# Optimization experiments

Hardware: AMD Instinct MI355X
Metric: run time of the kernel (lower is better)

## Reference

```python
import jax, jax.numpy as jnp
import numpy as np
from itertools import product

N_CODONS = 2
ORDER = 2
N_STATES = 25          # calc_number_of_states() with nCodons=2
ALPHA6 = 6             # alphabet_size + 2
OFFSET = 8 + 3 * N_CODONS       # 14, first insert state
TERM1 = OFFSET + 3 * (N_CODONS + 1)  # 23, terminal_1 state

CODE = {'A': [0], 'C': [1], 'G': [2], 'T': [3], 'N': [0, 1, 2, 3], 'X': [5]}


def _state_entries(state, emissions, x_must_preceed):
    ems = ['N'] * (ORDER - len(emissions) + 1) + list(emissions)[-(ORDER + 1):]
    allowed = [[state]]
    for i, e in enumerate(ems):
        allowed.append(CODE[e] + ([4] if i < ORDER - x_must_preceed else []))
    out = []
    for x in product(*allowed):
        found, ok = False, True
        for i in range(1, ORDER + 1):
            if found and x[i] == 4:
                ok = False
                break
            if x[i] != 4:
                found = True
        if ok:
            out.append(x)
    return out


def _emission_index_spec():
    entries, k = [], 0
    def add(state, ems, xp, trainable=True):
        nonlocal k
        ids = _state_entries(state, ems, xp)
        for t, x in enumerate(ids):
            entries.append((x, k + t if trainable else -1))
        if trainable:
            k += len(ids)
    add(0, 'N', 0); add(1, 'A', 0); add(2, 'AT', 0); add(3, 'ATG', 0, False)
    add(4, 'ATGN', 0); add(5, 'ATGNN', 0)
    for s in range(6, 6 + N_CODONS * 3 - 2):
        add(s, 'N', 0)
    add(4 + 3 * N_CODONS, 'T', ORDER)
    add(5 + 3 * N_CODONS, 'TA', ORDER); add(5 + 3 * N_CODONS, 'TG', ORDER)
    add(6 + 3 * N_CODONS, 'TAA', ORDER, False)
    add(6 + 3 * N_CODONS, 'TAG', ORDER, False)
    add(6 + 3 * N_CODONS, 'TGA', ORDER, False)
    add(7 + 3 * N_CODONS, 'N', ORDER)
    for s in range(8 + 3 * N_CODONS, 8 + 3 * N_CODONS + 3 * (N_CODONS + 1)):
        add(s, 'N', 0)
    for i in range(1, ORDER + 1):
        add(TERM1, 'X' * i, ORDER)
    add(TERM1 + 1, 'X' * (ORDER + 1), ORDER, False)
    idx = np.array([e[0] for e in entries], dtype=np.int32)
    widx = np.array([e[1] for e in entries], dtype=np.int32)
    return idx, widx

EM_IDX, EM_WIDX = _emission_index_spec()


def build_A(w):
    # sparse transition structure -> row-softmax over nonzeros -> dense [25,25]
    idx, vals = [], []
    def add(i, j, v):
        idx.append((i, j)); vals.append(v)
    n, k = N_CODONS, 0
    add(0, 0, 1 - w[k]); add(0, 1, w[k]); k += 1
    add(1, 2, 1.0); add(2, 3, 1.0)
    for i in range(n):
        add(3 + 3 * i, 4 + 3 * i, w[k + i])
    k += n
    for i in range(n):
        add(4 + 3 * i, 5 + 3 * i, 1.0)
    for i in range(n):
        add(5 + 3 * i, 6 + 3 * i, 1.0)
    for i in range(n + 1):
        add(3 + 3 * i, OFFSET + 3 * i, w[k + i])
    k += n + 1
    add(3 + 3 * n, 4 + 3 * n, 1 - w[k - 1])
    for i in range(n + 1):
        add(OFFSET + 3 * i, OFFSET + 1 + 3 * i, 1.0)
    for i in range(n + 1):
        add(OFFSET + 1 + 3 * i, OFFSET + 2 + 3 * i, 1.0)
    for i in range(n + 1):
        add(OFFSET + 2 + 3 * i, 4 + 3 * i, w[k + i])
    for i in range(n + 1):
        add(OFFSET + 2 + 3 * i, OFFSET + 3 * i, 1 - w[k + i])
    k += n + 1
    i_del = [3 + 3 * i for i in range(n) for _ in range(n - i)]
    j_del = [4 + 3 * j for i in range(1, n + 1) for j in range(i, n + 1)]
    for i, j in zip(i_del, j_del):
        add(i, j, 1 - w[k] * w[k] ** ((j - i) // 3))
    k += 1
    add(4 + 3 * n, 5 + 3 * n, 1.0); add(5 + 3 * n, 6 + 3 * n, 1.0)
    add(6 + 3 * n, 7 + 3 * n, 1.0)
    add(7 + 3 * n, 7 + 3 * n, 1.0); add(7 + 3 * n, TERM1, 1.0)
    add(TERM1, TERM1, 1.0); add(TERM1, TERM1 + 1, 1.0)
    add(TERM1 + 1, TERM1 + 1, 1.0)
    rows = np.array([i for i, _ in idx]); cols = np.array([j for _, j in idx])
    logits = jnp.stack([jnp.asarray(v, jnp.float32) for v in vals])
    M = jnp.full((N_STATES, N_STATES), -jnp.inf, jnp.float32).at[rows, cols].set(logits)
    A = jax.nn.softmax(M, axis=-1)
    return jnp.where(jnp.isfinite(M), A, 0.0)


def build_B(w):
    # sparse emission values (trainable weights or fixed 1), per-state softmax over nonzeros
    vals = jnp.where(EM_WIDX >= 0, w[np.clip(EM_WIDX, 0, None)], 1.0)
    rows = EM_IDX[:, 0]
    flat = EM_IDX[:, 1] * 36 + EM_IDX[:, 2] * 6 + EM_IDX[:, 3]
    M = jnp.full((N_STATES, ALPHA6 ** 3), -jnp.inf, jnp.float32).at[rows, flat].set(vals)
    B = jax.nn.softmax(M, axis=-1)
    return jnp.where(jnp.isfinite(M), B, 0.0)  # [25, 216]


def build_I(w):
    n_init = 3 + 3 * N_CODONS  # states 0..8 get initial mass
    p = jax.nn.softmax(w[:n_init])
    return jnp.zeros((N_STATES,), jnp.float32).at[:n_init].set(p)


def _forward(transition_kernel, emission_kernel, init_kernel, tokens):
    A = build_A(transition_kernel)
    Bf = build_B(emission_kernel)
    I = build_I(init_kernel)
    Bt, T = tokens.shape
    pad = jnp.full((Bt, ORDER), 4, tokens.dtype)  # '4' = no preceding emission
    tp = jnp.concatenate([pad, tokens], axis=1)
    flat = tp[:, :-2] * 36 + tp[:, 1:-1] * 6 + tp[:, 2:]  # [Bt, T]
    E = jnp.moveaxis(Bf.T[flat], 1, 0)  # [T, Bt, 25]
    alpha = I[None, :] * E[0]
    s = alpha.sum(-1, keepdims=True)
    alpha = alpha / s
    ll = jnp.log(s[..., 0])
    def step(carry, e):
        a, ll = carry
        a = (a @ A) * e
        s = a.sum(-1, keepdims=True)
        return (a / s, ll + jnp.log(s[..., 0])), None
    (alpha, ll), _ = jax.lax.scan(step, (alpha, ll), E[1:])
    return ll  # [Bt] per-sequence log-likelihood


def setup_inputs() -> dict:
    key = jax.random.key(0)
    k1, k2, k3, k4 = jax.random.split(key, 4)
    return {
        'transition_kernel': jax.random.normal(k1, (10,), jnp.float32) * 0.05,
        'emission_kernel': jax.random.normal(k2, (5400,), jnp.float32) * 0.05,
        'init_kernel': jax.random.normal(k3, (25,), jnp.float32) * 0.05,
        'tokens': jax.random.randint(k4, (512, 2048), 0, 4, jnp.int32),
    }


def reference(transition_kernel, emission_kernel, init_kernel, tokens):
    return _forward(transition_kernel, emission_kernel, init_kernel, tokens)
```

## Files before the change

kernel.cpp:

```cpp
#include <hip/hip_runtime.h>
#include <hip/hip_bf16.h>
#include <math.h>


typedef float v2f __attribute__((ext_vector_type(2)));
typedef float v4f __attribute__((ext_vector_type(4)));

#define NSTATES 25
#define NLIVE   23
#define NFLAT   216
#define NPACK   100
#define PITCH   28
#define TLEN    2048
#define NSEQ    512
#define CHUNKS  16
#define CLEN    128

#define LOG16 2.772588722239781f

__device__ __constant__ int PERMC[24] = {1,4,2,5,3,6,7,10,8,11,9,12,
                                         14,17,15,18,16,19,20,0,21,13,22,23};
__device__ __constant__ int POSA[NLIVE] = {19,0,2,4,1,3,5,6,8,10,7,9,11,21,
                                           12,14,16,13,15,17,18,20,22};

struct WMap { short m[NSTATES * NFLAT]; };

constexpr WMap make_wmap() {
  WMap w{};
  for (int i = 0; i < NSTATES * NFLAT; i++) w.m[i] = -2;
  const unsigned char ST[29] = {0,1,2,3,4,5,6,7,8,9,10,11,11,12,12,12,13,
                                14,15,16,17,18,19,20,21,22,23,23,24};
  const unsigned char M1[29] = {0x1F,0x1F,0x1F,0x11,0x18,0x14,0x1F,0x1F,0x1F,
                                0x1F,0x0F,0x0F,0x0F,0x08,0x08,0x08,0x0F,
                                0x1F,0x1F,0x1F,0x1F,0x1F,0x1F,0x1F,0x1F,0x1F,
                                0x0F,0x0F,0x20};
  const unsigned char M2[29] = {0x1F,0x1F,0x11,0x18,0x14,0x1F,0x1F,0x1F,0x1F,
                                0x1F,0x0F,0x08,0x08,0x01,0x01,0x04,0x0F,
                                0x1F,0x1F,0x1F,0x1F,0x1F,0x1F,0x1F,0x1F,0x1F,
                                0x0F,0x20,0x20};
  const unsigned char M3[29] = {0x0F,0x01,0x08,0x04,0x0F,0x0F,0x0F,0x0F,0x0F,
                                0x0F,0x08,0x01,0x04,0x01,0x04,0x01,0x0F,
                                0x0F,0x0F,0x0F,0x0F,0x0F,0x0F,0x0F,0x0F,0x0F,
                                0x20,0x20,0x20};
  const unsigned char TR[29] = {1,1,1,0,1,1,1,1,1,1,1,1,1,0,0,0,1,
                                1,1,1,1,1,1,1,1,1,1,1,0};
  int k = 0;
  for (int s = 0; s < 29; s++) {
    for (int c1 = 0; c1 < 6; c1++) {
      if (!((M1[s] >> c1) & 1)) continue;
      for (int c2 = 0; c2 < 6; c2++) {
        if (!((M2[s] >> c2) & 1)) continue;
        if (c1 != 4 && c2 == 4) continue;
        for (int c3 = 0; c3 < 6; c3++) {
          if (!((M3[s] >> c3) & 1)) continue;
          w.m[ST[s] * NFLAT + c1 * 36 + c2 * 6 + c3] =
              TR[s] ? (short)(k++) : (short)-1;
        }
      }
    }
  }
  return w;
}
__device__ __constant__ WMap WMAP = make_wmap();

__device__ __forceinline__ unsigned short f2bf(float x) {
  unsigned int u = __float_as_uint(x);
  u += 0x7fffu + ((u >> 16) & 1u);
  return (unsigned short)(u >> 16);
}

struct Wp2 {
  v2f w0, w1, w2, w3, w6, w7, w9, w10, w13, w14, w15, w16, w17, w18;
  float w4, w5, w8, w11;
};

#define SP(x) ((v2f){(x), (x)})
#define FMA2(a, ws, c) ((v2f){fmaf((a).x, (ws), (c).x), \
                              fmaf((a).y, (ws), (c).y)})

__device__ __forceinline__ void step_pk2(v2f (&Q)[23], const v4f (&F)[6],
                                         const Wp2& W) {
  v2f o19 = Q[19], o4 = Q[4], o5 = Q[5], o10 = Q[10], o11 = Q[11];
  v2f o21 = Q[21], o16 = Q[16], o17 = Q[17], o22 = Q[22];
  v2f o18 = Q[18], o20 = Q[20];

  v2f n0  = o19 * W.w0;
  v2f n1  = o19 * W.w1;
  v2f n4  = o4 * W.w2  + o16 * W.w13;
  v2f n14 = o4 * W.w3  + o16 * W.w14;
  v2f t77 = o5 * W.w6  + o17 * W.w15;
  v2f n7  = FMA2(o4, W.w4, t77);
  v2f n17 = o5 * W.w7  + o17 * W.w16;
  v2f tAA = o10 * W.w10 + o22 * W.w17;
  v2f n10 = FMA2(o4, W.w5, FMA2(o5, W.w8, tAA));
  v2f n20 = o10 * W.w9 + o22 * W.w18;
  v2f n13 = FMA2(o21, W.w11, o11);

  v2f s2  = Q[0]  * SP(F[0].z),  s3  = Q[1]  * SP(F[0].w);
  v2f s4  = Q[2]  * SP(F[1].x),  s5  = Q[3]  * SP(F[1].y);
  v2f s8  = Q[6]  * SP(F[2].x),  s9  = Q[7]  * SP(F[2].y);
  v2f s10 = Q[8]  * SP(F[2].z),  s11 = Q[9]  * SP(F[2].w);
  v2f s14 = Q[12] * SP(F[3].z),  s15 = Q[13] * SP(F[3].w);
  v2f s16 = Q[14] * SP(F[4].x),  s17 = Q[15] * SP(F[4].y);
  v2f s20 = o18 * SP(F[5].x);
  v2f s22 = o20 * SP(F[5].z);

  Q[0]  = n1  * SP(F[0].x);
  Q[1]  = n4  * SP(F[0].y);
  Q[6]  = n7  * SP(F[1].z);
  Q[7]  = n10 * SP(F[1].w);
  Q[12] = n14 * SP(F[3].x);
  Q[13] = n17 * SP(F[3].y);
  Q[18] = n20 * SP(F[4].z);
  Q[19] = n0  * SP(F[4].w);
  Q[20] = s20;
  Q[21] = n13 * SP(F[5].y);
  Q[22] = s22;
  Q[2] = s2;  Q[3] = s3;  Q[4] = s4;  Q[5] = s5;
  Q[8] = s8;  Q[9] = s9;  Q[10] = s10; Q[11] = s11;
  Q[14] = s14; Q[15] = s15; Q[16] = s16; Q[17] = s17;
}

__device__ __forceinline__ void renorm_pk2(v2f (&Q)[23], v2f& L) {
  v2f ax = (((Q[0] + Q[2]) + (Q[4] + Q[6])) +
            ((Q[8] + Q[10]) + (Q[12] + Q[14]))) +
           ((Q[16] + Q[18]) + (Q[20] + Q[22]));
  v2f ay = (((Q[1] + Q[3]) + (Q[5] + Q[7])) +
            ((Q[9] + Q[11]) + (Q[13] + Q[15]))) +
           ((Q[17] + Q[19]) + Q[21]);
  v2f s = ax + ay;
  bool okA = s.x > 0.0f, okB = s.y > 0.0f;
  L.x = okA ? L.x + __logf(s.x) : -3.0e38f;
  L.y = okB ? L.y + __logf(s.y) : -3.0e38f;
  v2f r;
  r.x = okA ? __fdividef(1.0f, s.x) : 1.0f;
  r.y = okB ? __fdividef(1.0f, s.y) : 1.0f;
  #pragma unroll
  for (int k = 0; k < 23; k++) Q[k] *= r;
}

#define LDROW(F, nt_) { int nt = (nt_); \
  const v4f* er = (const v4f*)(sBt + (((c12 << 2) + nt) * PITCH)); \
  F[0] = er[0]; F[1] = er[1]; F[2] = er[2]; \
  F[3] = er[3]; F[4] = er[4]; F[5] = er[5]; \
  c12 = p2 * 5 + nt; p2 = nt; }
#define LDSTEP(Fn, Fc, nt_) { LDROW(Fn, nt_); step_pk2(Q, Fc, W); }

__global__ __launch_bounds__(256)
void hmm_kernel(const float* __restrict__ wT, const float* __restrict__ wE,
                const float* __restrict__ wI, const int* __restrict__ tokens,
                float* __restrict__ out) {
  __shared__ __align__(16) float          sBt[NPACK * PITCH];
  __shared__ __align__(16) unsigned short sT[CHUNKS * NLIVE * 24];
  __shared__ float sL[CHUNKS * NLIVE];
  __shared__ float sAW[24];
  __shared__ float sI[32];

  const int tid   = threadIdx.x;
  const int seq   = blockIdx.x;
  const int chunk = tid >> 4;
  const int row16 = tid & 15;
  const int* trow = tokens + (size_t)seq * TLEN;

  {
    const int g32 = tid >> 5, r32 = tid & 31;
    for (int st = g32; st < NLIVE; st += 8) {
      const int pos = POSA[st];
      float part = 0.0f;
      for (int c = r32; c < NFLAT; c += 32) {
        short m = WMAP.m[st * NFLAT + c];
        if (m == -1) part += expf(1.0f);
        else if (m >= 0) part += expf(wE[m]);
      }
      #pragma unroll
      for (int m = 1; m < 32; m <<= 1) part += __shfl_xor(part, m, 32);
      float inv = 16.0f / part;
      for (int i = r32; i < NPACK; i += 32) {
        int c12 = i >> 2, nt = i & 3;
        int p1 = c12 / 5, p2v = c12 - 5 * p1;
        int flat = p1 * 36 + p2v * 6 + nt;
        short m = WMAP.m[st * NFLAT + flat];
        float v = 0.0f;
        if (m == -1) v = expf(1.0f);
        else if (m >= 0) v = expf(wE[m]);
        sBt[i * PITCH + pos] = v * inv;
      }
    }
  }
  for (int i = tid; i < NPACK; i += 256) sBt[i * PITCH + 23] = 0.0f;
  if (tid == 224) {
    const float w0 = wT[0], w1 = wT[1], w2 = wT[2], w3 = wT[3], w4 = wT[4];
    const float w5 = wT[5], w6 = wT[6], w7 = wT[7], w8 = wT[8], w9 = wT[9];
    { float e0 = expf(1.0f - w0), e1 = expf(w0), is = 1.0f / (e0 + e1);
      sAW[0] = e0 * is; sAW[1] = e1 * is; }
    { float e4 = expf(w1), e14 = expf(w3);
      float e7 = expf(1.0f - w9 * w9), e10 = expf(1.0f - w9 * w9 * w9);
      float is = 1.0f / (e4 + e14 + e7 + e10);
      sAW[2] = e4 * is;  sAW[3] = e14 * is;
      sAW[4] = e7 * is;  sAW[5] = e10 * is; }
    { float e7 = expf(w2), e17 = expf(w4), e10 = expf(1.0f - w9 * w9);
      float is = 1.0f / (e7 + e17 + e10);
      sAW[6] = e7 * is; sAW[7] = e17 * is; sAW[8] = e10 * is; }
    { float e20 = expf(w5), e10 = expf(1.0f - w5), is = 1.0f / (e20 + e10);
      sAW[9] = e20 * is; sAW[10] = e10 * is; }
    sAW[11] = 0.5f; sAW[12] = 0.5f;
    { float e4 = expf(w6), e14 = expf(1.0f - w6), is = 1.0f / (e4 + e14);
      sAW[13] = e4 * is; sAW[14] = e14 * is; }
    { float e7 = expf(w7), e17 = expf(1.0f - w7), is = 1.0f / (e7 + e17);
      sAW[15] = e7 * is; sAW[16] = e17 * is; }
    { float e10 = expf(w8), e20 = expf(1.0f - w8), is = 1.0f / (e10 + e20);
      sAW[17] = e10 * is; sAW[18] = e20 * is; }
    sAW[19] = 0.5f; sAW[20] = 0.5f;
  } else if (tid == 225) {
    float e[9], s = 0.0f;
    for (int i = 0; i < 9; i++) { e[i] = expf(wI[i]); s += e[i]; }
    float inv = 1.0f / s;
    for (int i = 0; i < 9; i++) sI[i] = e[i] * inv;
    for (int i = 9; i < 32; i++) sI[i] = 0.0f;
  }
  __syncthreads();

  float w[21];
  #pragma unroll
  for (int i = 0; i < 21; i++)
    w[i] = __uint_as_float(
        (unsigned)__builtin_amdgcn_readfirstlane(__float_as_uint(sAW[i])));
  Wp2 W;
  W.w0 = SP(w[0]);   W.w1 = SP(w[1]);   W.w2 = SP(w[2]);   W.w3 = SP(w[3]);
  W.w6 = SP(w[6]);   W.w7 = SP(w[7]);   W.w9 = SP(w[9]);   W.w10 = SP(w[10]);
  W.w13 = SP(w[13]); W.w14 = SP(w[14]); W.w15 = SP(w[15]); W.w16 = SP(w[16]);
  W.w17 = SP(w[17]); W.w18 = SP(w[18]);
  W.w4 = w[4]; W.w5 = w[5]; W.w8 = w[8]; W.w11 = w[11];

  const int t0 = chunk * CLEN;

  v2f Q[23];
  #pragma unroll
  for (int p = 0; p < 23; p++) {
    Q[p].x = (row16 == PERMC[p]) ? 1.0f : 0.0f;
    Q[p].y = (row16 + 16 == PERMC[p]) ? 1.0f : 0.0f;
  }
  v2f L = (v2f){0.0f, 0.0f};

  v4f FA[6], FB[6];
  int c12, p2;
  int4 q0 = *(const int4*)(trow + t0);
  int4 q1 = *(const int4*)(trow + t0 + 4);

  int b = 0;
  if (chunk == 0) {
    c12 = 20 + q0.x; p2 = q0.x;
    LDROW(FA, q0.y);
    LDSTEP(FB, FA, q0.z);
    LDSTEP(FA, FB, q0.w);
    LDSTEP(FB, FA, q1.x);
    LDSTEP(FA, FB, q1.y);
    LDSTEP(FB, FA, q1.z);
    LDSTEP(FA, FB, q1.w);
    step_pk2(Q, FA, W);
    b = 1;
    q0 = *(const int4*)(trow + 8);
    q1 = *(const int4*)(trow + 12);
  } else {
    int2 pp = *(const int2*)(trow + t0 - 2);
    c12 = pp.x * 5 + pp.y; p2 = pp.y;
  }

  for (; b < CLEN / 8; b++) {
    int4 n0 = q0, n1 = q1;
    if (b + 1 < CLEN / 8) {
      n0 = *(const int4*)(trow + t0 + (b + 1) * 8);
      n1 = *(const int4*)(trow + t0 + (b + 1) * 8 + 4);
    }
    LDROW(FA, q0.x);
    LDSTEP(FB, FA, q0.y);
    LDSTEP(FA, FB, q0.z);
    LDSTEP(FB, FA, q0.w);
    LDSTEP(FA, FB, q1.x);
    LDSTEP(FB, FA, q1.y);
    LDSTEP(FA, FB, q1.z);
    LDSTEP(FB, FA, q1.w);
    step_pk2(Q, FB, W);
    if (b & 1) renorm_pk2(Q, L);
    q0 = n0; q1 = n1;
  }

  const float undo = (chunk == 0 ? 127.0f : 128.0f) * LOG16;
  if (L.x > -1.0e38f) L.x -= undo;
  if (L.y > -1.0e38f) L.y -= undo;

  {
    const int baseA = (chunk * NLIVE + row16) * 24;
    #pragma unroll
    for (int k = 0; k < 12; k++) {
      ushort2 p;
      p.x = f2bf(Q[2 * k].x);
      p.y = (2 * k + 1 < 23) ? f2bf(Q[2 * k + 1].x) : (unsigned short)0;
      *(ushort2*)&sT[baseA + 2 * k] = p;
    }
    sL[chunk * NLIVE + row16] = L.x;
    if (row16 < 7) {
      const int baseB = (chunk * NLIVE + row16 + 16) * 24;
      #pragma unroll
      for (int k = 0; k < 12; k++) {
        ushort2 p;
        p.x = f2bf(Q[2 * k].y);
        p.y = (2 * k + 1 < 23) ? f2bf(Q[2 * k + 1].y) : (unsigned short)0;
        *(ushort2*)&sT[baseB + 2 * k] = p;
      }
      sL[chunk * NLIVE + row16 + 16] = L.y;
    }
  }
  __syncthreads();

  if (tid < 64) {
    const int lane = tid;
    const bool act = (lane < NLIVE);

    int jp = 23;
    #pragma unroll
    for (int pos = 0; pos < 23; pos++)
      if (PERMC[pos] == lane) jp = pos;

    const int tok0 = trow[0];
    const int idx0 = 96 + tok0;

    float v = act ? sI[lane] * sBt[idx0 * PITCH + jp] : 0.0f;
    float s = v;
    #pragma unroll
    for (int m = 1; m < 32; m <<= 1) s += __shfl_xor(s, m, 32);
    float ll = __logf(s) - LOG16;
    v = act ? v * __fdividef(1.0f, s) : 0.0f;

    for (int c = 0; c < CHUNKS; c++) {
      float Lj  = act ? sL[c * NLIVE + lane] : -3.0e38f;
      float key = (act && v > 0.0f) ? Lj : -3.0e38f;
      float mx = key;
      #pragma unroll
      for (int m = 1; m < 32; m <<= 1) mx = fmaxf(mx, __shfl_xor(mx, m, 32));
      float wgt = (act && v > 0.0f) ? v * __expf(Lj - mx) : 0.0f;

      float nv = 0.0f;
      #pragma unroll
      for (int r = 0; r < NLIVE; r++) {
        float wr = __shfl(wgt, r, 64);
        nv += wr * __uint_as_float(((unsigned)sT[(c * NLIVE + r) * 24 + jp]) << 16);
      }
      float nva = act ? nv : 0.0f;
      float s2 = nva;
      #pragma unroll
      for (int m = 1; m < 32; m <<= 1) s2 += __shfl_xor(s2, m, 32);
      ll += mx + __logf(s2);
      v = act ? nv * __fdividef(1.0f, s2) : 0.0f;
    }

    if (lane == 0) out[seq] = ll;
  }
}

extern "C" void kernel_launch(void* const* d_in, const int* in_sizes, int n_in,
                              void* d_out, int out_size, void* d_ws, size_t ws_size,
                              hipStream_t stream) {
  const float* wT = (const float*)d_in[0];
  const float* wE = (const float*)d_in[1];
  const float* wI = (const float*)d_in[2];
  const int* tokens = (const int*)d_in[3];
  float* out = (float*)d_out;
  (void)d_ws; (void)ws_size;

  hmm_kernel<<<NSEQ, 256, 0, stream>>>(wT, wE, wI, tokens, out);
}
```

Before: 122.2 us.

## Split each sequence into 32 chunks with four packed basis vectors per thread

The time axis of each sequence is now cut into 32 chunks of 64 steps instead of 16 chunks of 128. Each thread now carries four packed state-basis vectors (v4f) instead of two. The point is to halve the serial recurrence length per thread on a latency-bound scan, since each step now does twice as much independent packed math. In exchange, each thread holds more registers for Q, and the later chunk-combination phase has twice as many chunk matrices to merge.

```diff
diff --git a/kernel.cpp b/kernel.cpp
--- a/kernel.cpp
+++ b/kernel.cpp
@@ -3,7 +3,6 @@
 #include <math.h>
 
 
-typedef float v2f __attribute__((ext_vector_type(2)));
 typedef float v4f __attribute__((ext_vector_type(4)));
 
 #define NSTATES 25
@@ -13,8 +12,8 @@
 #define PITCH   28
 #define TLEN    2048
 #define NSEQ    512
-#define CHUNKS  16
-#define CLEN    128
+#define CHUNKS  32
+#define CLEN    64
 
 #define LOG16 2.772588722239781f
 
@@ -69,72 +68,75 @@
   return (unsigned short)(u >> 16);
 }
 
-struct Wp2 {
-  v2f w0, w1, w2, w3, w6, w7, w9, w10, w13, w14, w15, w16, w17, w18;
-  float w4, w5, w8, w11;
+struct Wp {
+  float w0, w1, w2, w3, w4, w5, w6, w7, w8, w9, w10, w11;
+  float w13, w14, w15, w16, w17, w18;
 };
 
-#define SP(x) ((v2f){(x), (x)})
-#define FMA2(a, ws, c) ((v2f){fmaf((a).x, (ws), (c).x), \
-                              fmaf((a).y, (ws), (c).y)})
-
-__device__ __forceinline__ void step_pk2(v2f (&Q)[23], const v4f (&F)[6],
-                                         const Wp2& W) {
-  v2f o19 = Q[19], o4 = Q[4], o5 = Q[5], o10 = Q[10], o11 = Q[11];
-  v2f o21 = Q[21], o16 = Q[16], o17 = Q[17], o22 = Q[22];
-  v2f o18 = Q[18], o20 = Q[20];
-
-  v2f n0  = o19 * W.w0;
-  v2f n1  = o19 * W.w1;
-  v2f n4  = o4 * W.w2  + o16 * W.w13;
-  v2f n14 = o4 * W.w3  + o16 * W.w14;
-  v2f t77 = o5 * W.w6  + o17 * W.w15;
-  v2f n7  = FMA2(o4, W.w4, t77);
-  v2f n17 = o5 * W.w7  + o17 * W.w16;
-  v2f tAA = o10 * W.w10 + o22 * W.w17;
-  v2f n10 = FMA2(o4, W.w5, FMA2(o5, W.w8, tAA));
-  v2f n20 = o10 * W.w9 + o22 * W.w18;
-  v2f n13 = FMA2(o21, W.w11, o11);
-
-  v2f s2  = Q[0]  * SP(F[0].z),  s3  = Q[1]  * SP(F[0].w);
-  v2f s4  = Q[2]  * SP(F[1].x),  s5  = Q[3]  * SP(F[1].y);
-  v2f s8  = Q[6]  * SP(F[2].x),  s9  = Q[7]  * SP(F[2].y);
-  v2f s10 = Q[8]  * SP(F[2].z),  s11 = Q[9]  * SP(F[2].w);
-  v2f s14 = Q[12] * SP(F[3].z),  s15 = Q[13] * SP(F[3].w);
-  v2f s16 = Q[14] * SP(F[4].x),  s17 = Q[15] * SP(F[4].y);
-  v2f s20 = o18 * SP(F[5].x);
-  v2f s22 = o20 * SP(F[5].z);
-
-  Q[0]  = n1  * SP(F[0].x);
-  Q[1]  = n4  * SP(F[0].y);
-  Q[6]  = n7  * SP(F[1].z);
-  Q[7]  = n10 * SP(F[1].w);
-  Q[12] = n14 * SP(F[3].x);
-  Q[13] = n17 * SP(F[3].y);
-  Q[18] = n20 * SP(F[4].z);
-  Q[19] = n0  * SP(F[4].w);
+#define S4(x) ((v4f){(x), (x), (x), (x)})
+#define FMA4(a, ws, c) ((v4f){fmaf((a).x, (ws), (c).x), \
+                              fmaf((a).y, (ws), (c).y), \
+                              fmaf((a).z, (ws), (c).z), \
+                              fmaf((a).w, (ws), (c).w)})
+
+__device__ __forceinline__ void step_pk4(v4f (&Q)[23], const v4f (&F)[6],
+                                         const Wp& W) {
+  v4f o19 = Q[19], o4 = Q[4], o5 = Q[5], o10 = Q[10], o11 = Q[11];
+  v4f o21 = Q[21], o16 = Q[16], o17 = Q[17], o22 = Q[22];
+  v4f o18 = Q[18], o20 = Q[20];
+
+  v4f n0  = o19 * S4(W.w0);
+  v4f n1  = o19 * S4(W.w1);
+  v4f n4  = o4 * S4(W.w2)  + o16 * S4(W.w13);
+  v4f n14 = o4 * S4(W.w3)  + o16 * S4(W.w14);
+  v4f t77 = o5 * S4(W.w6)  + o17 * S4(W.w15);
+  v4f n7  = FMA4(o4, W.w4, t77);
+  v4f n17 = o5 * S4(W.w7)  + o17 * S4(W.w16);
+  v4f tAA = o10 * S4(W.w10) + o22 * S4(W.w17);
+  v4f n10 = FMA4(o4, W.w5, FMA4(o5, W.w8, tAA));
+  v4f n20 = o10 * S4(W.w9) + o22 * S4(W.w18);
+  v4f n13 = FMA4(o21, W.w11, o11);
+
+  v4f s2  = Q[0]  * S4(F[0].z),  s3  = Q[1]  * S4(F[0].w);
+  v4f s4  = Q[2]  * S4(F[1].x),  s5  = Q[3]  * S4(F[1].y);
+  v4f s8  = Q[6]  * S4(F[2].x),  s9  = Q[7]  * S4(F[2].y);
+  v4f s10 = Q[8]  * S4(F[2].z),  s11 = Q[9]  * S4(F[2].w);
+  v4f s14 = Q[12] * S4(F[3].z),  s15 = Q[13] * S4(F[3].w);
+  v4f s16 = Q[14] * S4(F[4].x),  s17 = Q[15] * S4(F[4].y);
+  v4f s20 = o18 * S4(F[5].x);
+  v4f s22 = o20 * S4(F[5].z);
+
+  Q[0]  = n1  * S4(F[0].x);
+  Q[1]  = n4  * S4(F[0].y);
+  Q[6]  = n7  * S4(F[1].z);
+  Q[7]  = n10 * S4(F[1].w);
+  Q[12] = n14 * S4(F[3].x);
+  Q[13] = n17 * S4(F[3].y);
+  Q[18] = n20 * S4(F[4].z);
+  Q[19] = n0  * S4(F[4].w);
   Q[20] = s20;
-  Q[21] = n13 * SP(F[5].y);
+  Q[21] = n13 * S4(F[5].y);
   Q[22] = s22;
   Q[2] = s2;  Q[3] = s3;  Q[4] = s4;  Q[5] = s5;
   Q[8] = s8;  Q[9] = s9;  Q[10] = s10; Q[11] = s11;
   Q[14] = s14; Q[15] = s15; Q[16] = s16; Q[17] = s17;
 }
 
-__device__ __forceinline__ void renorm_pk2(v2f (&Q)[23], v2f& L) {
-  v2f ax = (((Q[0] + Q[2]) + (Q[4] + Q[6])) +
+__device__ __forceinline__ void renorm_pk4(v4f (&Q)[23], v4f& L) {
+  v4f ax = (((Q[0] + Q[2]) + (Q[4] + Q[6])) +
             ((Q[8] + Q[10]) + (Q[12] + Q[14]))) +
            ((Q[16] + Q[18]) + (Q[20] + Q[22]));
-  v2f ay = (((Q[1] + Q[3]) + (Q[5] + Q[7])) +
+  v4f ay = (((Q[1] + Q[3]) + (Q[5] + Q[7])) +
             ((Q[9] + Q[11]) + (Q[13] + Q[15]))) +
            ((Q[17] + Q[19]) + Q[21]);
-  v2f s = ax + ay;
-  bool okA = s.x > 0.0f, okB = s.y > 0.0f;
-  L.x = okA ? L.x + __logf(s.x) : -3.0e38f;
-  L.y = okB ? L.y + __logf(s.y) : -3.0e38f;
-  v2f r;
-  r.x = okA ? __fdividef(1.0f, s.x) : 1.0f;
-  r.y = okB ? __fdividef(1.0f, s.y) : 1.0f;
+  v4f s = ax + ay;
+  v4f r;
+  #pragma unroll
+  for (int h = 0; h < 4; h++) {
+    bool ok = s[h] > 0.0f;
+    L[h] = ok ? L[h] + __logf(s[h]) : -3.0e38f;
+    r[h] = ok ? __fdividef(1.0f, s[h]) : 1.0f;
+  }
   #pragma unroll
   for (int k = 0; k < 23; k++) Q[k] *= r;
 }
@@ -144,7 +146,7 @@
   F[0] = er[0]; F[1] = er[1]; F[2] = er[2]; \
   F[3] = er[3]; F[4] = er[4]; F[5] = er[5]; \
   c12 = p2 * 5 + nt; p2 = nt; }
-#define LDSTEP(Fn, Fc, nt_) { LDROW(Fn, nt_); step_pk2(Q, Fc, W); }
+#define LDSTEP(Fn, Fc, nt_) { LDROW(Fn, nt_); step_pk4(Q, Fc, W); }
 
 __global__ __launch_bounds__(256)
 void hmm_kernel(const float* __restrict__ wT, const float* __restrict__ wE,
@@ -158,8 +160,8 @@
 
   const int tid   = threadIdx.x;
   const int seq   = blockIdx.x;
-  const int chunk = tid >> 4;
-  const int row16 = tid & 15;
+  const int chunk = tid >> 3;
+  const int row8  = tid & 7;
   const int* trow = tokens + (size_t)seq * TLEN;
 
   {
@@ -225,22 +227,24 @@
   for (int i = 0; i < 21; i++)
     w[i] = __uint_as_float(
         (unsigned)__builtin_amdgcn_readfirstlane(__float_as_uint(sAW[i])));
-  Wp2 W;
-  W.w0 = SP(w[0]);   W.w1 = SP(w[1]);   W.w2 = SP(w[2]);   W.w3 = SP(w[3]);
-  W.w6 = SP(w[6]);   W.w7 = SP(w[7]);   W.w9 = SP(w[9]);   W.w10 = SP(w[10]);
-  W.w13 = SP(w[13]); W.w14 = SP(w[14]); W.w15 = SP(w[15]); W.w16 = SP(w[16]);
-  W.w17 = SP(w[17]); W.w18 = SP(w[18]);
-  W.w4 = w[4]; W.w5 = w[5]; W.w8 = w[8]; W.w11 = w[11];
+  Wp W;
+  W.w0 = w[0];   W.w1 = w[1];   W.w2 = w[2];   W.w3 = w[3];
+  W.w4 = w[4];   W.w5 = w[5];   W.w6 = w[6];   W.w7 = w[7];
+  W.w8 = w[8];   W.w9 = w[9];   W.w10 = w[10]; W.w11 = w[11];
+  W.w13 = w[13]; W.w14 = w[14]; W.w15 = w[15]; W.w16 = w[16];
+  W.w17 = w[17]; W.w18 = w[18];
 
   const int t0 = chunk * CLEN;
 
-  v2f Q[23];
+  v4f Q[23];
   #pragma unroll
   for (int p = 0; p < 23; p++) {
-    Q[p].x = (row16 == PERMC[p]) ? 1.0f : 0.0f;
-    Q[p].y = (row16 + 16 == PERMC[p]) ? 1.0f : 0.0f;
-  }
-  v2f L = (v2f){0.0f, 0.0f};
+    Q[p] = (v4f){ (row8      == PERMC[p]) ? 1.0f : 0.0f,
+                  (row8 + 8  == PERMC[p]) ? 1.0f : 0.0f,
+                  (row8 + 16 == PERMC[p]) ? 1.0f : 0.0f,
+                  (row8 + 24 == PERMC[p]) ? 1.0f : 0.0f };
+  }
+  v4f L = (v4f){0.0f, 0.0f, 0.0f, 0.0f};
 
   v4f FA[6], FB[6];
   int c12, p2;
@@ -257,7 +261,7 @@
     LDSTEP(FA, FB, q1.y);
     LDSTEP(FB, FA, q1.z);
     LDSTEP(FA, FB, q1.w);
-    step_pk2(Q, FA, W);
+    step_pk4(Q, FA, W);
     b = 1;
     q0 = *(const int4*)(trow + 8);
     q1 = *(const int4*)(trow + 12);
@@ -280,35 +284,29 @@
     LDSTEP(FB, FA, q1.y);
     LDSTEP(FA, FB, q1.z);
     LDSTEP(FB, FA, q1.w);
-    step_pk2(Q, FB, W);
-    if (b & 1) renorm_pk2(Q, L);
+    step_pk4(Q, FB, W);
+    if (b & 1) renorm_pk4(Q, L);
     q0 = n0; q1 = n1;
   }
 
-  const float undo = (chunk == 0 ? 127.0f : 128.0f) * LOG16;
-  if (L.x > -1.0e38f) L.x -= undo;
-  if (L.y > -1.0e38f) L.y -= undo;
-
-  {
-    const int baseA = (chunk * NLIVE + row16) * 24;
-    #pragma unroll
-    for (int k = 0; k < 12; k++) {
-      ushort2 p;
-      p.x = f2bf(Q[2 * k].x);
-      p.y = (2 * k + 1 < 23) ? f2bf(Q[2 * k + 1].x) : (unsigned short)0;
-      *(ushort2*)&sT[baseA + 2 * k] = p;
-    }
-    sL[chunk * NLIVE + row16] = L.x;
-    if (row16 < 7) {
-      const int baseB = (chunk * NLIVE + row16 + 16) * 24;
+  const float undo = (chunk == 0 ? 63.0f : 64.0f) * LOG16;
+  #pragma unroll
+  for (int h = 0; h < 4; h++)
+    if (L[h] > -1.0e38f) L[h] -= undo;
+
+  #pragma unroll
+  for (int h = 0; h < 4; h++) {
+    const int bs = row8 + 8 * h;
+    if (bs < 23) {
+      const int base = (chunk * NLIVE + bs) * 24;
       #pragma unroll
       for (int k = 0; k < 12; k++) {
         ushort2 p;
-        p.x = f2bf(Q[2 * k].y);
-        p.y = (2 * k + 1 < 23) ? f2bf(Q[2 * k + 1].y) : (unsigned short)0;
-        *(ushort2*)&sT[baseB + 2 * k] = p;
-      }
-      sL[chunk * NLIVE + row16 + 16] = L.y;
+        p.x = f2bf(Q[2 * k][h]);
+        p.y = (2 * k + 1 < 23) ? f2bf(Q[2 * k + 1][h]) : (unsigned short)0;
+        *(ushort2*)&sT[base + 2 * k] = p;
+      }
+      sL[chunk * NLIVE + bs] = L[h];
     }
   }
   __syncthreads();
```

Result: slower. 174.8 us (+43.1%).
